# Performance work log

Measured on AMD Instinct MI355X. Metric: run time of the kernel, lower is better.

Reference implementation:

```python
import jax, jax.numpy as jnp
import numpy as np

N_HEADS = 16
D_MODEL = 1024
D_K = 64
D_V = 64
LN_EPS = 1e-6


def setup_inputs() -> dict:
    key = jax.random.key(0)
    ks = jax.random.split(key, 16)
    B, L, D = 4, 512, D_MODEL
    s = 1.0 / np.sqrt(D)
    return {
        "q": jax.random.normal(ks[0], (B, L, D), jnp.float32),
        "k": jax.random.normal(ks[1], (B, L, D), jnp.float32),
        "v": jax.random.normal(ks[2], (B, L, D), jnp.float32),
        "bias": jax.random.normal(ks[3], (B, N_HEADS, L, L), jnp.float32),
        "graph_attn_bias": jax.random.normal(ks[4], (B, N_HEADS, L, L), jnp.float32),
        # projection weights stored as [in, out] (math-equivalent to torch Linear)
        "wq": jax.random.normal(ks[5], (D, N_HEADS * D_K), jnp.float32) * s,
        "bq": jnp.zeros((N_HEADS * D_K,), jnp.float32),
        "wk": jax.random.normal(ks[6], (D, N_HEADS * D_K), jnp.float32) * s,
        "bk": jnp.zeros((N_HEADS * D_K,), jnp.float32),
        "wv": jax.random.normal(ks[7], (D, N_HEADS * D_V), jnp.float32) * s,
        "bv": jnp.zeros((N_HEADS * D_V,), jnp.float32),
        "wo": jax.random.normal(ks[8], (N_HEADS * D_V, D), jnp.float32) * s,
        "bo": jnp.zeros((D,), jnp.float32),
        "ln_g": jnp.ones((D,), jnp.float32),
        "ln_b": jnp.zeros((D,), jnp.float32),
    }


def reference(q, k, v, bias, graph_attn_bias, wq, bq, wk, bk, wv, bv, wo, bo, ln_g, ln_b):
    B, Lq, D = q.shape
    H, dk, dv = N_HEADS, D_K, D_V
    residual = q
    # fused QKV projections, split heads -> [B, H, L, d]
    qh = (q @ wq + bq).reshape(B, Lq, H, dk).transpose(0, 2, 1, 3)
    kh = (k @ wk + bk).reshape(B, k.shape[1], H, dk).transpose(0, 2, 1, 3)
    vh = (v @ wv + bv).reshape(B, v.shape[1], H, dv).transpose(0, 2, 1, 3)
    # graph scaled dot-product attention: scores + mask bias + structural bias
    scores = jnp.einsum("bhqd,bhkd->bhqk", qh / np.sqrt(dk).astype(qh.dtype), kh)
    scores = scores + bias + graph_attn_bias
    weights = jax.nn.softmax(scores, axis=-1)
    ctx = jnp.einsum("bhqk,bhkd->bhqd", weights, vh)  # [B,H,Lq,dv]
    ctx = ctx.transpose(0, 2, 1, 3).reshape(B, Lq, H * dv)
    out = ctx @ wo + bo + residual
    # LayerNorm(eps=1e-6)
    mu = jnp.mean(out, axis=-1, keepdims=True)
    var = jnp.var(out, axis=-1, keepdims=True)
    out = (out - mu) * jax.lax.rsqrt(var + LN_EPS) * ln_g + ln_b
    return out
```

## Files before the change

kernel.cpp:

```cpp
#include <hip/hip_runtime.h>

#define D_MODEL 1024
#define N_HEADS 16
#define DK 64
#define LSEQ 512
#define BATCH 4
#define M_ROWS (BATCH * LSEQ)

typedef unsigned short ushort_t;
typedef __attribute__((ext_vector_type(8))) short short8;
typedef __attribute__((ext_vector_type(4))) float floatx4;

__device__ __forceinline__ float bf2f(unsigned short u) {
    return __uint_as_float(((unsigned int)u) << 16);
}
__device__ __forceinline__ unsigned short f2bf(float f) {
    unsigned int u = __float_as_uint(f);
    u += 0x7fffu + ((u >> 16) & 1u);
    return (unsigned short)(u >> 16);
}

__global__ __launch_bounds__(256) void cast3_kernel(
    const float* __restrict__ a, const float* __restrict__ b,
    const float* __restrict__ c, ushort_t* __restrict__ oa,
    ushort_t* __restrict__ ob, ushort_t* __restrict__ oc, int n)
{
    const float* src = (blockIdx.y == 0) ? a : (blockIdx.y == 1) ? b : c;
    ushort_t* dst = (blockIdx.y == 0) ? oa : (blockIdx.y == 1) ? ob : oc;
    int i = (blockIdx.x * 256 + threadIdx.x) * 4;
    if (i + 3 < n) {
        float4 v = *(const float4*)(src + i);
        ushort4 o = make_ushort4(f2bf(v.x), f2bf(v.y), f2bf(v.z), f2bf(v.w));
        *(ushort4*)(dst + i) = o;
    }
}

__global__ __launch_bounds__(256) void transpose4_kernel(
    const float* __restrict__ w0, const float* __restrict__ w1,
    const float* __restrict__ w2, const float* __restrict__ w3,
    ushort_t* __restrict__ o0, ushort_t* __restrict__ o1,
    ushort_t* __restrict__ o2, ushort_t* __restrict__ o3)
{
    __shared__ float tile[32][33];
    const float* W = (blockIdx.z == 0) ? w0 : (blockIdx.z == 1) ? w1
                   : (blockIdx.z == 2) ? w2 : w3;
    ushort_t* O = (blockIdx.z == 0) ? o0 : (blockIdx.z == 1) ? o1
                : (blockIdx.z == 2) ? o2 : o3;
    const int tx = threadIdx.x & 31;
    const int ty = threadIdx.x >> 5;
    const int kbase = blockIdx.y * 32;
    const int nbase = blockIdx.x * 32;
    #pragma unroll
    for (int j = 0; j < 4; ++j)
        tile[ty + 8 * j][tx] = W[(size_t)(kbase + ty + 8 * j) * 1024 + nbase + tx];
    __syncthreads();
    #pragma unroll
    for (int j = 0; j < 4; ++j) {
        int n = nbase + ty + 8 * j;
        O[(size_t)n * 1024 + kbase + tx] = f2bf(tile[tx][ty + 8 * j]);
    }
}

template <bool OUT_BF16, bool ADD_BVEC, bool ADD_RES>
__device__ __forceinline__ void gemm_bt_body(
    const ushort_t* __restrict__ A, const ushort_t* __restrict__ Bt,
    const float* __restrict__ bvec, const float* __restrict__ res,
    void* __restrict__ outp, int N, int K, int kStart, int kEnd,
    int rowBase, int colBase, ushort_t* As, ushort_t* Bs)
{
    const int tid = threadIdx.x;
    const int l = tid & 63;
    const int w = tid >> 6;
    const int wave_m = w >> 1;
    const int wave_n = w & 1;

    const int srow8 = l >> 3;
    const int cgl = ((l & 7) + srow8) & 7;
    const ushort_t* gA0 = A  + (size_t)(rowBase + w * 16 + 0 + srow8) * K + cgl * 8;
    const ushort_t* gA1 = A  + (size_t)(rowBase + w * 16 + 8 + srow8) * K + cgl * 8;
    const ushort_t* gB0 = Bt + (size_t)(colBase + w * 16 + 0 + srow8) * K + cgl * 8;
    const ushort_t* gB1 = Bt + (size_t)(colBase + w * 16 + 8 + srow8) * K + cgl * 8;
    ushort_t* lA0 = As + w * 1024;
    ushort_t* lA1 = As + w * 1024 + 512;
    ushort_t* lB0 = Bs + w * 1024;
    ushort_t* lB1 = Bs + w * 1024 + 512;

    floatx4 acc[2][2];
    #pragma unroll
    for (int i = 0; i < 2; ++i)
        #pragma unroll
        for (int j = 0; j < 2; ++j)
            acc[i][j] = (floatx4){0.f, 0.f, 0.f, 0.f};

    const int fm = l & 15;
    const int fg = l >> 4;

    for (int k0 = kStart; k0 < kEnd; k0 += 64) {
        __builtin_amdgcn_global_load_lds(
            (const __attribute__((address_space(1))) void*)(gA0 + k0),
            (__attribute__((address_space(3))) void*)lA0, 16, 0, 0);
        __builtin_amdgcn_global_load_lds(
            (const __attribute__((address_space(1))) void*)(gA1 + k0),
            (__attribute__((address_space(3))) void*)lA1, 16, 0, 0);
        __builtin_amdgcn_global_load_lds(
            (const __attribute__((address_space(1))) void*)(gB0 + k0),
            (__attribute__((address_space(3))) void*)lB0, 16, 0, 0);
        __builtin_amdgcn_global_load_lds(
            (const __attribute__((address_space(1))) void*)(gB1 + k0),
            (__attribute__((address_space(3))) void*)lB1, 16, 0, 0);
        __syncthreads();

        short8 afrag[2][2], bfrag[2][2];
        #pragma unroll
        for (int mi = 0; mi < 2; ++mi)
            #pragma unroll
            for (int kt = 0; kt < 2; ++kt) {
                int p = ((kt * 4 + fg) - fm) & 7;
                afrag[mi][kt] = *(const short8*)
                    &As[(wave_m * 32 + mi * 16 + fm) * 64 + p * 8];
            }
        #pragma unroll
        for (int ni = 0; ni < 2; ++ni)
            #pragma unroll
            for (int kt = 0; kt < 2; ++kt) {
                int p = ((kt * 4 + fg) - fm) & 7;
                bfrag[ni][kt] = *(const short8*)
                    &Bs[(wave_n * 32 + ni * 16 + fm) * 64 + p * 8];
            }

        #pragma unroll
        for (int kt = 0; kt < 2; ++kt)
            #pragma unroll
            for (int mi = 0; mi < 2; ++mi)
                #pragma unroll
                for (int ni = 0; ni < 2; ++ni)
                    acc[mi][ni] = __builtin_amdgcn_mfma_f32_16x16x32_bf16(
                        afrag[mi][kt], bfrag[ni][kt], acc[mi][ni], 0, 0, 0);
        __syncthreads();
    }

    const int crow0 = rowBase + wave_m * 32 + fg * 4;
    const int ccol0 = colBase + wave_n * 32 + fm;
    #pragma unroll
    for (int mi = 0; mi < 2; ++mi) {
        #pragma unroll
        for (int ni = 0; ni < 2; ++ni) {
            const int col = ccol0 + ni * 16;
            const float bb = ADD_BVEC ? bvec[col] : 0.f;
            #pragma unroll
            for (int r = 0; r < 4; ++r) {
                const int row = crow0 + mi * 16 + r;
                float v = acc[mi][ni][r] + bb;
                if (ADD_RES) v += res[(size_t)row * N + col];
                if (OUT_BF16)
                    ((ushort_t*)outp)[(size_t)row * N + col] = f2bf(v);
                else
                    ((float*)outp)[(size_t)row * N + col] = v;
            }
        }
    }
}

__global__ __launch_bounds__(256) void gemm_qkv(
    const ushort_t* a0, const ushort_t* a1, const ushort_t* a2,
    const ushort_t* t0, const ushort_t* t1, const ushort_t* t2,
    const float* b0, const float* b1, const float* b2,
    ushort_t* o0, ushort_t* o1, ushort_t* o2)
{
    __shared__ ushort_t As[64 * 64];
    __shared__ ushort_t Bs[64 * 64];
    const int z = blockIdx.z;
    const ushort_t* A  = (z == 0) ? a0 : (z == 1) ? a1 : a2;
    const ushort_t* Bt = (z == 0) ? t0 : (z == 1) ? t1 : t2;
    const float* bv    = (z == 0) ? b0 : (z == 1) ? b1 : b2;
    ushort_t* o        = (z == 0) ? o0 : (z == 1) ? o1 : o2;
    gemm_bt_body<true, true, false>(A, Bt, bv, nullptr, o, D_MODEL, D_MODEL,
                                    0, D_MODEL,
                                    blockIdx.y * 64, blockIdx.x * 64, As, Bs);
}

__global__ __launch_bounds__(256) void gemm_out(
    const ushort_t* __restrict__ A, const ushort_t* __restrict__ Bt,
    const float* __restrict__ bvec, const float* __restrict__ res,
    float* __restrict__ out0, float* __restrict__ out1)
{
    __shared__ ushort_t As[64 * 64];
    __shared__ ushort_t Bs[64 * 64];
    if (blockIdx.z == 0)
        gemm_bt_body<false, true, true>(A, Bt, bvec, res, out0, D_MODEL,
                                        D_MODEL, 0, 512,
                                        blockIdx.y * 64, blockIdx.x * 64, As, Bs);
    else
        gemm_bt_body<false, false, false>(A, Bt, nullptr, nullptr, out1, D_MODEL,
                                          D_MODEL, 512, 1024,
                                          blockIdx.y * 64, blockIdx.x * 64, As, Bs);
}

__global__ __launch_bounds__(256) void attn_mfma(
    const ushort_t* __restrict__ qh, const ushort_t* __restrict__ kh,
    const ushort_t* __restrict__ vh, const float* __restrict__ bias,
    const float* __restrict__ gbias, ushort_t* __restrict__ ctx)
{
    __shared__ ushort_t Qs[16 * 72];
    __shared__ float S[16 * 516];
    __shared__ float Vt[64 * 36];
    __shared__ float red[16][17];
    __shared__ float rowmax[16];
    __shared__ float rowinv[16];

    const int tid = threadIdx.x;
    const int l = tid & 63;
    const int w = tid >> 6;
    const int m = l & 15;
    const int g = l >> 4;

    const int bh = blockIdx.y;
    const int h = bh & (N_HEADS - 1);
    const int b = bh >> 4;
    const int q0 = blockIdx.x * 16;

    const ushort_t* Qg = qh + ((size_t)(b * LSEQ + q0)) * D_MODEL + h * DK;
    const ushort_t* Kg = kh + ((size_t)(b * LSEQ)) * D_MODEL + h * DK;
    const ushort_t* Vg = vh + ((size_t)(b * LSEQ)) * D_MODEL + h * DK;

    if (tid < 128) {
        int row = tid >> 3, seg = tid & 7;
        short8 t = *(const short8*)(Qg + (size_t)row * D_MODEL + seg * 8);
        *(short8*)&Qs[row * 72 + seg * 8] = t;
    }
    __syncthreads();

    short8 aq0 = *(const short8*)&Qs[m * 72 + g * 8];
    short8 aq1 = *(const short8*)&Qs[m * 72 + g * 8 + 32];

    #pragma unroll 2
    for (int it = 0; it < 8; ++it) {
        const int kb = it * 64 + w * 16;
        const ushort_t* kr = Kg + (size_t)(kb + m) * D_MODEL + g * 8;
        short8 bk0 = *(const short8*)kr;
        short8 bk1 = *(const short8*)(kr + 32);
        floatx4 acc = (floatx4){0.f, 0.f, 0.f, 0.f};
        acc = __builtin_amdgcn_mfma_f32_16x16x32_bf16(aq0, bk0, acc, 0, 0, 0);
        acc = __builtin_amdgcn_mfma_f32_16x16x32_bf16(aq1, bk1, acc, 0, 0, 0);
        const int col = kb + m;
        const int qrow0 = g * 4;
        #pragma unroll
        for (int r = 0; r < 4; ++r)
            S[(qrow0 + r) * 516 + col] = acc[r] * 0.125f;
    }
    __syncthreads();

    {
        const int row = tid >> 4, s = tid & 15;
        float* Srow = &S[row * 516];
        const float* bp = bias  + ((size_t)bh * LSEQ + q0 + row) * LSEQ;
        const float* gp = gbias + ((size_t)bh * LSEQ + q0 + row) * LSEQ;

        float4 vv[8];
        float mx = -1e30f;
        #pragma unroll
        for (int i = 0; i < 8; ++i) {
            const int col = 4 * s + 64 * i;
            float4 sv = *(const float4*)&Srow[col];
            float4 bb = *(const float4*)(bp + col);
            float4 gg = *(const float4*)(gp + col);
            float4 v = make_float4(sv.x + bb.x + gg.x, sv.y + bb.y + gg.y,
                                   sv.z + bb.z + gg.z, sv.w + bb.w + gg.w);
            vv[i] = v;
            mx = fmaxf(mx, fmaxf(fmaxf(v.x, v.y), fmaxf(v.z, v.w)));
        }
        red[row][s] = mx;
        __syncthreads();
        if (tid < 16) {
            float mm = red[tid][0];
            #pragma unroll
            for (int c = 1; c < 16; ++c) mm = fmaxf(mm, red[tid][c]);
            rowmax[tid] = mm;
        }
        __syncthreads();
        mx = rowmax[row];

        float sum = 0.f;
        unsigned* Pd = (unsigned*)Srow;
        #pragma unroll
        for (int i = 0; i < 8; ++i) {
            float e0 = __expf(vv[i].x - mx);
            float e1 = __expf(vv[i].y - mx);
            float e2 = __expf(vv[i].z - mx);
            float e3 = __expf(vv[i].w - mx);
            sum += (e0 + e1) + (e2 + e3);
            Pd[2 * s + 32 * i]     = (unsigned)f2bf(e0) | ((unsigned)f2bf(e1) << 16);
            Pd[2 * s + 32 * i + 1] = (unsigned)f2bf(e2) | ((unsigned)f2bf(e3) << 16);
        }
        red[row][s] = sum;
        __syncthreads();
        if (tid < 16) {
            float t = 0.f;
            #pragma unroll
            for (int c = 0; c < 16; ++c) t += red[tid][c];
            rowinv[tid] = 1.0f / t;
        }
    }

    const ushort_t* Ps = (const ushort_t*)S;
    floatx4 oacc = (floatx4){0.f, 0.f, 0.f, 0.f};
    const unsigned* VtD = (const unsigned*)Vt;

    for (int vt = 0; vt < 8; ++vt) {
        const int kv0 = vt * 64;
        __syncthreads();
        {
            const int kp = tid & 31, dg = tid >> 5;
            const ushort_t* vr = Vg + (size_t)(kv0 + 2 * kp) * D_MODEL + dg * 8;
            short8 r0 = *(const short8*)vr;
            short8 r1 = *(const short8*)(vr + D_MODEL);
            unsigned* vtp = (unsigned*)Vt;
            #pragma unroll
            for (int i = 0; i < 8; ++i) {
                unsigned dwv = (unsigned)(ushort_t)r0[i]
                             | ((unsigned)(ushort_t)r1[i] << 16);
                vtp[(dg * 8 + i) * 36 + kp] = dwv;
            }
        }
        __syncthreads();
        #pragma unroll
        for (int kt = 0; kt < 2; ++kt) {
            short8 pf = *(const short8*)&Ps[(size_t)m * 1032 + kv0 + kt * 32 + g * 8];
            short8 vf = *(const short8*)&VtD[(w * 16 + m) * 36 + kt * 16 + g * 4];
            oacc = __builtin_amdgcn_mfma_f32_16x16x32_bf16(pf, vf, oacc, 0, 0, 0);
        }
    }

    {
        const int qrow0 = g * 4;
        const int dcol = w * 16 + m;
        ushort_t* cp = ctx + ((size_t)(b * LSEQ + q0 + qrow0)) * D_MODEL + h * DK + dcol;
        #pragma unroll
        for (int r = 0; r < 4; ++r)
            cp[(size_t)r * D_MODEL] = f2bf(oacc[r] * rowinv[qrow0 + r]);
    }
}

__global__ __launch_bounds__(256) void ln_kernel(
    float* __restrict__ x, const float* __restrict__ part2,
    const float* __restrict__ g, const float* __restrict__ beta)
{
    const int row = blockIdx.x;
    float* xr = x + (size_t)row * D_MODEL;
    const float* pr = part2 + (size_t)row * D_MODEL;
    const int tid = threadIdx.x;

    float v[4];
    float s = 0.f, sq = 0.f;
    #pragma unroll
    for (int j = 0; j < 4; ++j) {
        v[j] = xr[tid + 256 * j] + pr[tid + 256 * j];
        s += v[j];
        sq += v[j] * v[j];
    }
    __shared__ float rs[256], rq[256];
    rs[tid] = s;
    rq[tid] = sq;
    __syncthreads();
    for (int st = 128; st > 0; st >>= 1) {
        if (tid < st) { rs[tid] += rs[tid + st]; rq[tid] += rq[tid + st]; }
        __syncthreads();
    }
    const float mean = rs[0] * (1.0f / D_MODEL);
    const float var = rq[0] * (1.0f / D_MODEL) - mean * mean;
    const float rinv = rsqrtf(var + 1e-6f);
    #pragma unroll
    for (int j = 0; j < 4; ++j) {
        int n = tid + 256 * j;
        xr[n] = (v[j] - mean) * rinv * g[n] + beta[n];
    }
}

extern "C" void kernel_launch(void* const* d_in, const int* in_sizes, int n_in,
                              void* d_out, int out_size, void* d_ws, size_t ws_size,
                              hipStream_t stream)
{
    const float* q     = (const float*)d_in[0];
    const float* k     = (const float*)d_in[1];
    const float* v     = (const float*)d_in[2];
    const float* bias  = (const float*)d_in[3];
    const float* gbias = (const float*)d_in[4];
    const float* wq    = (const float*)d_in[5];
    const float* bq    = (const float*)d_in[6];
    const float* wk    = (const float*)d_in[7];
    const float* bk    = (const float*)d_in[8];
    const float* wv    = (const float*)d_in[9];
    const float* bv    = (const float*)d_in[10];
    const float* wo    = (const float*)d_in[11];
    const float* bo    = (const float*)d_in[12];
    const float* ln_g  = (const float*)d_in[13];
    const float* ln_b  = (const float*)d_in[14];

    const size_t MB = 1u << 20;
    char* wsb = (char*)d_ws;
    ushort_t* vb   = (ushort_t*)(wsb + 0 * MB);
    ushort_t* wqb  = (ushort_t*)(wsb + 4 * MB);
    ushort_t* wkb  = (ushort_t*)(wsb + 6 * MB);
    ushort_t* wvb  = (ushort_t*)(wsb + 8 * MB);
    ushort_t* wob  = (ushort_t*)(wsb + 10 * MB);
    ushort_t* qhb  = (ushort_t*)(wsb + 12 * MB);
    ushort_t* khb  = (ushort_t*)(wsb + 16 * MB);
    ushort_t* vhb  = (ushort_t*)(wsb + 20 * MB);
    ushort_t* ctxb = (ushort_t*)(wsb + 24 * MB);
    float* out1 = (float*)(wsb + 12 * MB);
    ushort_t* qb = (ushort_t*)d_out;
    ushort_t* kb = (ushort_t*)d_out + (size_t)M_ROWS * D_MODEL;
    float* outp = (float*)d_out;

    const int NELEM = M_ROWS * D_MODEL;

    cast3_kernel<<<dim3(NELEM / 1024, 3), 256, 0, stream>>>(
        q, k, v, qb, kb, vb, NELEM);
    transpose4_kernel<<<dim3(32, 32, 4), 256, 0, stream>>>(
        wq, wk, wv, wo, wqb, wkb, wvb, wob);

    dim3 gqkv(D_MODEL / 64, M_ROWS / 64, 3);
    gemm_qkv<<<gqkv, 256, 0, stream>>>(
        qb, kb, vb, wqb, wkb, wvb, bq, bk, bv, qhb, khb, vhb);

    dim3 ablk(LSEQ / 16, BATCH * N_HEADS);
    attn_mfma<<<ablk, 256, 0, stream>>>(qhb, khb, vhb, bias, gbias, ctxb);

    dim3 gout(D_MODEL / 64, M_ROWS / 64, 2);
    gemm_out<<<gout, 256, 0, stream>>>(ctxb, wob, bo, q, outp, out1);

    ln_kernel<<<M_ROWS, 256, 0, stream>>>(outp, out1, ln_g, ln_b);
}
```

Baseline: 273.5 us.

## Keep attention scores in registers and softmax via wave shuffles in attn_mfma

The attention kernel now keeps the QK^T MFMA accumulators for all eight key tiles in registers. It adds the bias and graph bias directly in the MFMA output layout and computes row max and sum with cross-lane shuffles plus a small per-wave reduction in shared memory. This removes the fp32 score buffer in LDS and several barrier-separated reduction passes, leaving only a compact bf16 P buffer, which cuts LDS use and is meant to raise occupancy (launch bounds now request 4 blocks). The trade-offs are higher register pressure and bias loads that are scalar and strided per lane rather than float4-coalesced.

```diff
diff --git a/kernel.cpp b/kernel.cpp
--- a/kernel.cpp
+++ b/kernel.cpp
@@ -196,17 +196,16 @@
                                           blockIdx.y * 64, blockIdx.x * 64, As, Bs);
 }
 
-__global__ __launch_bounds__(256) void attn_mfma(
+__global__ __launch_bounds__(256, 4) void attn_mfma(
     const ushort_t* __restrict__ qh, const ushort_t* __restrict__ kh,
     const ushort_t* __restrict__ vh, const float* __restrict__ bias,
     const float* __restrict__ gbias, ushort_t* __restrict__ ctx)
 {
-    __shared__ ushort_t Qs[16 * 72];
-    __shared__ float S[16 * 516];
+    __shared__ __attribute__((aligned(16))) ushort_t Qs[16 * 72];
+    __shared__ __attribute__((aligned(16))) ushort_t P[16 * 520];
     __shared__ float Vt[64 * 36];
-    __shared__ float red[16][17];
-    __shared__ float rowmax[16];
-    __shared__ float rowinv[16];
+    __shared__ float redm[4][16];
+    __shared__ float reds[4][16];
 
     const int tid = threadIdx.x;
     const int l = tid & 63;
@@ -233,76 +232,82 @@
     short8 aq0 = *(const short8*)&Qs[m * 72 + g * 8];
     short8 aq1 = *(const short8*)&Qs[m * 72 + g * 8 + 32];
 
-    #pragma unroll 2
+    floatx4 acc[8];
+    #pragma unroll
     for (int it = 0; it < 8; ++it) {
         const int kb = it * 64 + w * 16;
         const ushort_t* kr = Kg + (size_t)(kb + m) * D_MODEL + g * 8;
         short8 bk0 = *(const short8*)kr;
         short8 bk1 = *(const short8*)(kr + 32);
-        floatx4 acc = (floatx4){0.f, 0.f, 0.f, 0.f};
-        acc = __builtin_amdgcn_mfma_f32_16x16x32_bf16(aq0, bk0, acc, 0, 0, 0);
-        acc = __builtin_amdgcn_mfma_f32_16x16x32_bf16(aq1, bk1, acc, 0, 0, 0);
-        const int col = kb + m;
-        const int qrow0 = g * 4;
+        floatx4 a = (floatx4){0.f, 0.f, 0.f, 0.f};
+        a = __builtin_amdgcn_mfma_f32_16x16x32_bf16(aq0, bk0, a, 0, 0, 0);
+        a = __builtin_amdgcn_mfma_f32_16x16x32_bf16(aq1, bk1, a, 0, 0, 0);
+        acc[it] = a;
+    }
+
+    const float* bp = bias  + ((size_t)bh * LSEQ + q0) * LSEQ + w * 16 + m;
+    const float* gp = gbias + ((size_t)bh * LSEQ + q0) * LSEQ + w * 16 + m;
+    float bsum[8][4];
+    #pragma unroll
+    for (int it = 0; it < 8; ++it)
+        #pragma unroll
+        for (int r = 0; r < 4; ++r) {
+            const size_t off = (size_t)(g * 4 + r) * LSEQ + it * 64;
+            bsum[it][r] = bp[off] + gp[off];
+        }
+    #pragma unroll
+    for (int it = 0; it < 8; ++it)
         #pragma unroll
         for (int r = 0; r < 4; ++r)
-            S[(qrow0 + r) * 516 + col] = acc[r] * 0.125f;
+            acc[it][r] = acc[it][r] * 0.125f + bsum[it][r];
+
+    float mx[4];
+    #pragma unroll
+    for (int r = 0; r < 4; ++r) {
+        float pm = fmaxf(
+            fmaxf(fmaxf(acc[0][r], acc[1][r]), fmaxf(acc[2][r], acc[3][r])),
+            fmaxf(fmaxf(acc[4][r], acc[5][r]), fmaxf(acc[6][r], acc[7][r])));
+        #pragma unroll
+        for (int d = 1; d < 16; d <<= 1)
+            pm = fmaxf(pm, __shfl_xor(pm, d, 64));
+        mx[r] = pm;
+    }
+    if (m == 0) {
+        #pragma unroll
+        for (int r = 0; r < 4; ++r) redm[w][g * 4 + r] = mx[r];
     }
     __syncthreads();
-
-    {
-        const int row = tid >> 4, s = tid & 15;
-        float* Srow = &S[row * 516];
-        const float* bp = bias  + ((size_t)bh * LSEQ + q0 + row) * LSEQ;
-        const float* gp = gbias + ((size_t)bh * LSEQ + q0 + row) * LSEQ;
-
-        float4 vv[8];
-        float mx = -1e30f;
-        #pragma unroll
-        for (int i = 0; i < 8; ++i) {
-            const int col = 4 * s + 64 * i;
-            float4 sv = *(const float4*)&Srow[col];
-            float4 bb = *(const float4*)(bp + col);
-            float4 gg = *(const float4*)(gp + col);
-            float4 v = make_float4(sv.x + bb.x + gg.x, sv.y + bb.y + gg.y,
-                                   sv.z + bb.z + gg.z, sv.w + bb.w + gg.w);
-            vv[i] = v;
-            mx = fmaxf(mx, fmaxf(fmaxf(v.x, v.y), fmaxf(v.z, v.w)));
+    #pragma unroll
+    for (int r = 0; r < 4; ++r)
+        mx[r] = fmaxf(fmaxf(redm[0][g * 4 + r], redm[1][g * 4 + r]),
+                      fmaxf(redm[2][g * 4 + r], redm[3][g * 4 + r]));
+
+    float sm[4] = {0.f, 0.f, 0.f, 0.f};
+    #pragma unroll
+    for (int it = 0; it < 8; ++it)
+        #pragma unroll
+        for (int r = 0; r < 4; ++r) {
+            float e = __expf(acc[it][r] - mx[r]);
+            sm[r] += e;
+            P[(g * 4 + r) * 520 + it * 64 + w * 16 + m] = f2bf(e);
         }
-        red[row][s] = mx;
-        __syncthreads();
-        if (tid < 16) {
-            float mm = red[tid][0];
-            #pragma unroll
-            for (int c = 1; c < 16; ++c) mm = fmaxf(mm, red[tid][c]);
-            rowmax[tid] = mm;
-        }
-        __syncthreads();
-        mx = rowmax[row];
-
-        float sum = 0.f;
-        unsigned* Pd = (unsigned*)Srow;
-        #pragma unroll
-        for (int i = 0; i < 8; ++i) {
-            float e0 = __expf(vv[i].x - mx);
-            float e1 = __expf(vv[i].y - mx);
-            float e2 = __expf(vv[i].z - mx);
-            float e3 = __expf(vv[i].w - mx);
-            sum += (e0 + e1) + (e2 + e3);
-            Pd[2 * s + 32 * i]     = (unsigned)f2bf(e0) | ((unsigned)f2bf(e1) << 16);
-            Pd[2 * s + 32 * i + 1] = (unsigned)f2bf(e2) | ((unsigned)f2bf(e3) << 16);
-        }
-        red[row][s] = sum;
-        __syncthreads();
-        if (tid < 16) {
-            float t = 0.f;
-            #pragma unroll
-            for (int c = 0; c < 16; ++c) t += red[tid][c];
-            rowinv[tid] = 1.0f / t;
-        }
-    }
-
-    const ushort_t* Ps = (const ushort_t*)S;
+    #pragma unroll
+    for (int r = 0; r < 4; ++r) {
+        #pragma unroll
+        for (int d = 1; d < 16; d <<= 1)
+            sm[r] += __shfl_xor(sm[r], d, 64);
+    }
+    if (m == 0) {
+        #pragma unroll
+        for (int r = 0; r < 4; ++r) reds[w][g * 4 + r] = sm[r];
+    }
+    __syncthreads();
+    float rinv[4];
+    #pragma unroll
+    for (int r = 0; r < 4; ++r)
+        rinv[r] = 1.0f / (reds[0][g * 4 + r] + reds[1][g * 4 + r] +
+                          reds[2][g * 4 + r] + reds[3][g * 4 + r]);
+
     floatx4 oacc = (floatx4){0.f, 0.f, 0.f, 0.f};
     const unsigned* VtD = (const unsigned*)Vt;
 
@@ -325,7 +330,7 @@
         __syncthreads();
         #pragma unroll
         for (int kt = 0; kt < 2; ++kt) {
-            short8 pf = *(const short8*)&Ps[(size_t)m * 1032 + kv0 + kt * 32 + g * 8];
+            short8 pf = *(const short8*)&P[(size_t)m * 520 + kv0 + kt * 32 + g * 8];
             short8 vf = *(const short8*)&VtD[(w * 16 + m) * 36 + kt * 16 + g * 4];
             oacc = __builtin_amdgcn_mfma_f32_16x16x32_bf16(pf, vf, oacc, 0, 0, 0);
         }
@@ -337,7 +342,7 @@
         ushort_t* cp = ctx + ((size_t)(b * LSEQ + q0 + qrow0)) * D_MODEL + h * DK + dcol;
         #pragma unroll
         for (int r = 0; r < 4; ++r)
-            cp[(size_t)r * D_MODEL] = f2bf(oacc[r] * rowinv[qrow0 + r]);
+            cp[(size_t)r * D_MODEL] = f2bf(oacc[r] * rinv[r]);
     }
 }
 
```

After: 270.2 us. Within noise of the previous version (-1.2%).
